# Optimization experiments

Hardware: AMD Instinct MI355X
Metric: run time of the kernel (lower is better)

Reference implementation:

```python
import jax, jax.numpy as jnp
import numpy as np


def _gcn_conv(x, W, b, src, dst, n):
    # x: [N, F_in] -> project first (dense GEMM), then normalized scatter-add.
    h = x @ W  # [N, F_out]
    deg = jax.ops.segment_sum(jnp.ones_like(dst, dtype=h.dtype), dst, num_segments=n)  # in-degree incl. self loops
    inv_sqrt = jax.lax.rsqrt(deg)  # deg >= 1 because self loops were added
    norm = inv_sqrt[src] * inv_sqrt[dst]  # [E+N]
    out = jax.ops.segment_sum(h[src] * norm[:, None], dst, num_segments=n)  # [N, F_out]
    return out + b


def setup_inputs() -> dict:
    key = jax.random.key(0)
    k1, k2, k3, k4 = jax.random.split(key, 4)
    N, E, F_IN, H, C = 10000, 160000, 3703, 1024, 6
    x = jax.random.normal(k1, (N, F_IN), dtype=jnp.float32)
    edge_index = jax.random.randint(k2, (2, E), 0, N, dtype=jnp.int64)
    # Glorot-style init for weights
    W1 = jax.random.normal(k3, (F_IN, H), dtype=jnp.float32) * np.float32(1.0 / np.sqrt(F_IN))
    W2 = jax.random.normal(k4, (H, C), dtype=jnp.float32) * np.float32(1.0 / np.sqrt(H))
    b1 = jnp.zeros((H,), dtype=jnp.float32)
    b2 = jnp.zeros((C,), dtype=jnp.float32)
    return {"x": x, "edge_index": edge_index, "W1": W1, "b1": b1, "W2": W2, "b2": b2}


def reference(x, edge_index, W1, b1, W2, b2):
    n = x.shape[0]
    # GCNConv adds self loops; degree normalization D^{-1/2}(A+I)D^{-1/2}
    loop = jnp.arange(n, dtype=edge_index.dtype)
    src = jnp.concatenate([edge_index[0], loop])
    dst = jnp.concatenate([edge_index[1], loop])
    h = _gcn_conv(x, W1, b1, src, dst, n)
    h = jax.nn.relu(h)
    # dropout is identity in eval mode
    h = _gcn_conv(h, W2, b2, src, dst, n)
    return jax.nn.log_softmax(h, axis=1)
```

## Files before the change

### kernel.cpp

```cpp
#include <hip/hip_runtime.h>
#include <stdint.h>

typedef unsigned short u16;
typedef unsigned int u32;
typedef __bf16 bf16x8 __attribute__((ext_vector_type(8)));
typedef float f32x4 __attribute__((ext_vector_type(4)));

#define N_NODES 10000
#define N_EDGES 160000
#define F_IN    3703
#define HDIM    1024
#define CDIM    6
#define MP      10112
#define KP      3712
#define KT      58

static __device__ __forceinline__ u16 f2bf(float f) {
    u32 u = __builtin_bit_cast(u32, f);
    u32 r = (u + 0x7fffu + ((u >> 16) & 1u)) >> 16;
    return (u16)r;
}
static __device__ __forceinline__ float bf2f(u16 b) {
    return __builtin_bit_cast(float, ((u32)b) << 16);
}

#define GL2LDS(g, l) __builtin_amdgcn_global_load_lds(                         \
    (const __attribute__((address_space(1))) void*)(g),                        \
    (__attribute__((address_space(3))) void*)(l), 16, 0, 0)

__global__ void k_count(const int* __restrict__ ei, int* counts) {
    int e = blockIdx.x * 256 + threadIdx.x;
    if (e < N_EDGES) {
        int dst = ei[N_EDGES + e];
        atomicAdd(&counts[dst], 1);
    }
}

__global__ void k_scan(const int* __restrict__ counts, int* __restrict__ offsets,
                       float* __restrict__ inv_sqrt) {
    __shared__ int sums[1024];
    int t = threadIdx.x;
    int local[10];
    int s = 0;
    #pragma unroll
    for (int i = 0; i < 10; i++) {
        int idx = t * 10 + i;
        int v = (idx < N_NODES) ? counts[idx] : 0;
        local[i] = s; s += v;
    }
    sums[t] = s;
    __syncthreads();
    for (int off = 1; off < 1024; off <<= 1) {
        int v = (t >= off) ? sums[t - off] : 0;
        __syncthreads();
        sums[t] += v;
        __syncthreads();
    }
    int base = (t == 0) ? 0 : sums[t - 1];
    #pragma unroll
    for (int i = 0; i < 10; i++) {
        int idx = t * 10 + i;
        if (idx < N_NODES) {
            offsets[idx] = base + local[i];
            inv_sqrt[idx] = rsqrtf((float)(counts[idx] + 1));
        }
    }
    if (t == 1023) offsets[N_NODES] = sums[1023];
}

__global__ void k_fill(const int* __restrict__ ei, const int* __restrict__ offsets,
                       int* cursor, int* __restrict__ edge_src) {
    int e = blockIdx.x * 256 + threadIdx.x;
    if (e < N_EDGES) {
        int src = ei[e];
        int dst = ei[N_EDGES + e];
        int pos = atomicAdd(&cursor[dst], 1);
        edge_src[offsets[dst] + pos] = src;
    }
}

__global__ void k_cvt_x(const float* __restrict__ x, u16* __restrict__ A) {
    const int KP4 = KP / 4;
    int i = blockIdx.x * 256 + threadIdx.x;
    if (i >= MP * KP4) return;
    int m = i / KP4;
    int k4 = (i - m * KP4) * 4;
    float v0 = 0.f, v1 = 0.f, v2 = 0.f, v3 = 0.f;
    if (m < N_NODES) {
        const float* xp = x + (size_t)m * F_IN;
        if (k4 + 3 < F_IN) {
            v0 = xp[k4]; v1 = xp[k4 + 1]; v2 = xp[k4 + 2]; v3 = xp[k4 + 3];
        } else {
            if (k4     < F_IN) v0 = xp[k4];
            if (k4 + 1 < F_IN) v1 = xp[k4 + 1];
            if (k4 + 2 < F_IN) v2 = xp[k4 + 2];
            if (k4 + 3 < F_IN) v3 = xp[k4 + 3];
        }
    }
    ushort4 o;
    o.x = f2bf(v0); o.y = f2bf(v1); o.z = f2bf(v2); o.w = f2bf(v3);
    *(ushort4*)&A[(size_t)m * KP + k4] = o;
}

__global__ void k_cvt_w1t(const float* __restrict__ W1, u16* __restrict__ BT) {
    __shared__ u16 tile[64][66];
    int k0 = blockIdx.x * 64, n0 = blockIdx.y * 64;
    int tx = threadIdx.x & 63, ty = threadIdx.x >> 6;
    #pragma unroll
    for (int i = 0; i < 16; i++) {
        int kk = ty + i * 4;
        int k = k0 + kk;
        float v = (k < F_IN) ? W1[(size_t)k * HDIM + n0 + tx] : 0.f;
        tile[kk][tx] = f2bf(v);
    }
    __syncthreads();
    #pragma unroll
    for (int i = 0; i < 16; i++) {
        int nn = ty + i * 4;
        BT[(size_t)(n0 + nn) * KP + k0 + tx] = tile[tx][nn];
    }
}

__global__ __launch_bounds__(256) void k_gemm1(const u16* __restrict__ A,
                                               const u16* __restrict__ BT,
                                               u16* __restrict__ H1) {
    __shared__ __align__(16) u16 As[128 * 64];
    __shared__ __align__(16) u16 Bs[128 * 64];
    const int tid = threadIdx.x;
    const int lane = tid & 63;
    const int wid = tid >> 6;
    const int wm = wid >> 1, wn = wid & 1;

    const u32 orig = (u32)blockIdx.y * 8u + (u32)blockIdx.x;
    const u32 lin  = (orig & 7u) * 79u + (orig >> 3);
    const int bm = (int)(lin >> 3);
    const int bn = (int)(lin & 7u);

    int srow[4], scol[4], sdst[4];
    #pragma unroll
    for (int j = 0; j < 4; j++) {
        int q = wid * 4 + j;
        int e = q * 512 + lane * 8;
        int row = e >> 6, c = e & 63;
        srow[j] = row;
        scol[j] = c ^ ((row & 7) << 3);
        sdst[j] = q * 512;
    }
    const u16* Abase = A + (size_t)bm * 128 * KP;
    const u16* Bbase = BT + (size_t)bn * 128 * KP;

    f32x4 acc[4][4];
    #pragma unroll
    for (int i = 0; i < 4; i++)
        #pragma unroll
        for (int j = 0; j < 4; j++)
            acc[i][j] = (f32x4)0.f;

    for (int kt = 0; kt < KT; ++kt) {
        const int k0 = kt * 64;
        #pragma unroll
        for (int j = 0; j < 4; j++)
            GL2LDS(Abase + srow[j] * KP + k0 + scol[j], As + sdst[j]);
        #pragma unroll
        for (int j = 0; j < 4; j++)
            GL2LDS(Bbase + srow[j] * KP + k0 + scol[j], Bs + sdst[j]);
        __syncthreads();

        const int rA = wm * 64 + (lane & 15);
        const int rB = wn * 64 + (lane & 15);
        const int cb = (lane >> 4) << 3;
        #pragma unroll
        for (int kk = 0; kk < 2; kk++) {
            bf16x8 av[4], bv[4];
            const int cc = kk * 32 + cb;
            #pragma unroll
            for (int i = 0; i < 4; i++) {
                int r = rA + i * 16;
                av[i] = *(const bf16x8*)(As + r * 64 + (cc ^ ((r & 7) << 3)));
                int r2 = rB + i * 16;
                bv[i] = *(const bf16x8*)(Bs + r2 * 64 + (cc ^ ((r2 & 7) << 3)));
            }
            #pragma unroll
            for (int i = 0; i < 4; i++)
                #pragma unroll
                for (int j = 0; j < 4; j++)
                    acc[i][j] = __builtin_amdgcn_mfma_f32_16x16x32_bf16(
                        av[i], bv[j], acc[i][j], 0, 0, 0);
        }
        __syncthreads();
    }

    const int cr = (lane >> 4) * 4;
    const int ccol = lane & 15;
    #pragma unroll
    for (int i = 0; i < 4; i++) {
        #pragma unroll
        for (int j = 0; j < 4; j++) {
            #pragma unroll
            for (int r = 0; r < 4; r++) {
                int row = bm * 128 + wm * 64 + i * 16 + cr + r;
                if (row < N_NODES) {
                    int col = bn * 128 + wn * 64 + j * 16 + ccol;
                    H1[(size_t)row * HDIM + col] = f2bf(acc[i][j][r]);
                }
            }
        }
    }
}

__global__ void k_agg1g2(const u16* __restrict__ H1, const int* __restrict__ offsets,
                         const int* __restrict__ edge_src, const float* __restrict__ inv_sqrt,
                         const float* __restrict__ b1, const float* __restrict__ W2,
                         float* __restrict__ H2) {
    __shared__ float red[4][8];
    int node = blockIdx.x;
    int t = threadIdx.x;
    int f = t * 4;
    float is_n = inv_sqrt[node];
    float a0, a1, a2, a3;
    {
        float w = is_n * is_n;
        ushort4 v = *(const ushort4*)(H1 + (size_t)node * HDIM + f);
        a0 = bf2f(v.x) * w; a1 = bf2f(v.y) * w; a2 = bf2f(v.z) * w; a3 = bf2f(v.w) * w;
    }
    int beg = offsets[node], end = offsets[node + 1];
    for (int e = beg; e < end; ++e) {
        int s = edge_src[e];
        float w = inv_sqrt[s] * is_n;
        ushort4 v = *(const ushort4*)(H1 + (size_t)s * HDIM + f);
        a0 += bf2f(v.x) * w; a1 += bf2f(v.y) * w; a2 += bf2f(v.z) * w; a3 += bf2f(v.w) * w;
    }
    float4 bb = *(const float4*)(b1 + f);
    float z0 = fmaxf(a0 + bb.x, 0.f);
    float z1 = fmaxf(a1 + bb.y, 0.f);
    float z2 = fmaxf(a2 + bb.z, 0.f);
    float z3 = fmaxf(a3 + bb.w, 0.f);
    float acc[6];
    #pragma unroll
    for (int c = 0; c < 6; c++)
        acc[c] = z0 * W2[(size_t)f * 6 + c] + z1 * W2[(size_t)(f + 1) * 6 + c]
               + z2 * W2[(size_t)(f + 2) * 6 + c] + z3 * W2[(size_t)(f + 3) * 6 + c];
    #pragma unroll
    for (int c = 0; c < 6; c++) {
        #pragma unroll
        for (int off = 32; off > 0; off >>= 1) acc[c] += __shfl_xor(acc[c], off);
    }
    int lane = t & 63, wv = t >> 6;
    if (lane == 0) {
        #pragma unroll
        for (int c = 0; c < 6; c++) red[wv][c] = acc[c];
    }
    __syncthreads();
    if (t < 6) {
        float s = red[0][t] + red[1][t] + red[2][t] + red[3][t];
        H2[(size_t)node * CDIM + t] = s;
    }
}

__global__ void k_agg2(const float* __restrict__ H2, const int* __restrict__ offsets,
                       const int* __restrict__ edge_src, const float* __restrict__ inv_sqrt,
                       const float* __restrict__ b2, float* __restrict__ out) {
    int gt = blockIdx.x * 256 + threadIdx.x;
    int node = gt >> 3, sub = gt & 7;
    if (node >= N_NODES) return;
    float is_n = inv_sqrt[node];
    float acc[6] = {0.f, 0.f, 0.f, 0.f, 0.f, 0.f};
    int beg = offsets[node], end = offsets[node + 1];
    for (int e = beg + sub; e < end; e += 8) {
        int s = edge_src[e];
        float w = inv_sqrt[s] * is_n;
        #pragma unroll
        for (int c = 0; c < 6; c++) acc[c] += H2[(size_t)s * CDIM + c] * w;
    }
    if (sub == 0) {
        float w = is_n * is_n;
        #pragma unroll
        for (int c = 0; c < 6; c++) acc[c] += H2[(size_t)node * CDIM + c] * w;
    }
    #pragma unroll
    for (int off = 1; off < 8; off <<= 1) {
        #pragma unroll
        for (int c = 0; c < 6; c++) acc[c] += __shfl_xor(acc[c], off);
    }
    if (sub == 0) {
        float z[6];
        #pragma unroll
        for (int c = 0; c < 6; c++) z[c] = acc[c] + b2[c];
        float m = z[0];
        #pragma unroll
        for (int c = 1; c < 6; c++) m = fmaxf(m, z[c]);
        float ssum = 0.f;
        #pragma unroll
        for (int c = 0; c < 6; c++) ssum += __expf(z[c] - m);
        float l = m + logf(ssum);
        #pragma unroll
        for (int c = 0; c < 6; c++) out[(size_t)node * CDIM + c] = z[c] - l;
    }
}

extern "C" void kernel_launch(void* const* d_in, const int* in_sizes, int n_in,
                              void* d_out, int out_size, void* d_ws, size_t ws_size,
                              hipStream_t stream) {
    const float* x  = (const float*)d_in[0];
    const int*   ei = (const int*)d_in[1];
    const float* W1 = (const float*)d_in[2];
    const float* b1 = (const float*)d_in[3];
    const float* W2 = (const float*)d_in[4];
    const float* b2 = (const float*)d_in[5];
    float* out = (float*)d_out;

    char* ws = (char*)d_ws;
    size_t off = 0;
    auto alloc = [&](size_t bytes) -> void* {
        void* p = ws + off;
        off += (bytes + 255) & ~(size_t)255;
        return p;
    };
    u16* A        = (u16*)alloc((size_t)MP * KP * 2);
    u16* BT       = (u16*)alloc((size_t)HDIM * KP * 2);
    u16* H1       = (u16*)alloc((size_t)N_NODES * HDIM * 2);
    int* counts   = (int*)alloc(N_NODES * 4);
    int* cursor   = (int*)alloc(N_NODES * 4);
    int* offsets  = (int*)alloc((N_NODES + 1) * 4);
    float* inv_sq = (float*)alloc(N_NODES * 4);
    int* edge_src = (int*)alloc(N_EDGES * 4);
    float* H2 = (float*)BT;

    hipMemsetAsync(counts, 0, N_NODES * 4, stream);
    hipMemsetAsync(cursor, 0, N_NODES * 4, stream);
    k_count<<<(N_EDGES + 255) / 256, 256, 0, stream>>>(ei, counts);
    k_scan<<<1, 1024, 0, stream>>>(counts, offsets, inv_sq);
    k_fill<<<(N_EDGES + 255) / 256, 256, 0, stream>>>(ei, offsets, cursor, edge_src);

    k_cvt_x<<<(MP * (KP / 4) + 255) / 256, 256, 0, stream>>>(x, A);
    dim3 gT(KP / 64, HDIM / 64);
    k_cvt_w1t<<<gT, 256, 0, stream>>>(W1, BT);

    dim3 gG(HDIM / 128, MP / 128);
    k_gemm1<<<gG, 256, 0, stream>>>(A, BT, H1);

    k_agg1g2<<<N_NODES, 256, 0, stream>>>(H1, offsets, edge_src, inv_sq, b1, W2, H2);
    k_agg2<<<(N_NODES * 8 + 255) / 256, 256, 0, stream>>>(H2, offsets, edge_src, inv_sq, b2, out);
}
```

Measured before the change: 240.1 us.

## Fuse fp32-to-bf16 conversion of x into GEMM with double-buffered LDS pipeline

Drops the separate pass that converts x to padded bf16. The GEMM now loads fp32 x directly into registers, converts it, and writes it into a double-buffered LDS tile. The next k-tile's A and B loads are issued before the current tile's MFMAs, so global latency overlaps with compute. The block scan is rewritten to use wavefront shuffles instead of a barrier-heavy LDS Hillis-Steele scan. In exchange, fp32 A loads are unaligned (F_IN is odd), use more registers and double LDS use, which may lower occupancy, and x is re-read by all 8 column blocks at fp32 width.

After: 287.5 us. 19.7% more time.

```diff
diff --git a/kernel.cpp b/kernel.cpp
--- a/kernel.cpp
+++ b/kernel.cpp
@@ -5,13 +5,13 @@
 typedef unsigned int u32;
 typedef __bf16 bf16x8 __attribute__((ext_vector_type(8)));
 typedef float f32x4 __attribute__((ext_vector_type(4)));
+typedef float f32x4u __attribute__((ext_vector_type(4), aligned(4)));
 
 #define N_NODES 10000
 #define N_EDGES 160000
 #define F_IN    3703
 #define HDIM    1024
 #define CDIM    6
-#define MP      10112
 #define KP      3712
 #define KT      58
 
@@ -38,8 +38,8 @@
 
 __global__ void k_scan(const int* __restrict__ counts, int* __restrict__ offsets,
                        float* __restrict__ inv_sqrt) {
-    __shared__ int sums[1024];
-    int t = threadIdx.x;
+    __shared__ int wsum[16];
+    int t = threadIdx.x, lane = t & 63, wv = t >> 6;
     int local[10];
     int s = 0;
     #pragma unroll
@@ -48,15 +48,21 @@
         int v = (idx < N_NODES) ? counts[idx] : 0;
         local[i] = s; s += v;
     }
-    sums[t] = s;
-    __syncthreads();
-    for (int off = 1; off < 1024; off <<= 1) {
-        int v = (t >= off) ? sums[t - off] : 0;
-        __syncthreads();
-        sums[t] += v;
-        __syncthreads();
-    }
-    int base = (t == 0) ? 0 : sums[t - 1];
+    int incl = s;
+    #pragma unroll
+    for (int off = 1; off < 64; off <<= 1) {
+        int v = __shfl_up(incl, off);
+        if (lane >= off) incl += v;
+    }
+    if (lane == 63) wsum[wv] = incl;
+    __syncthreads();
+    if (t == 0) {
+        int a = 0;
+        #pragma unroll
+        for (int i = 0; i < 16; i++) { int v = wsum[i]; wsum[i] = a; a += v; }
+    }
+    __syncthreads();
+    int base = wsum[wv] + incl - s;
     #pragma unroll
     for (int i = 0; i < 10; i++) {
         int idx = t * 10 + i;
@@ -65,7 +71,7 @@
             inv_sqrt[idx] = rsqrtf((float)(counts[idx] + 1));
         }
     }
-    if (t == 1023) offsets[N_NODES] = sums[1023];
+    if (t == 1023) offsets[N_NODES] = wsum[15] + incl;
 }
 
 __global__ void k_fill(const int* __restrict__ ei, const int* __restrict__ offsets,
@@ -79,29 +85,6 @@
     }
 }
 
-__global__ void k_cvt_x(const float* __restrict__ x, u16* __restrict__ A) {
-    const int KP4 = KP / 4;
-    int i = blockIdx.x * 256 + threadIdx.x;
-    if (i >= MP * KP4) return;
-    int m = i / KP4;
-    int k4 = (i - m * KP4) * 4;
-    float v0 = 0.f, v1 = 0.f, v2 = 0.f, v3 = 0.f;
-    if (m < N_NODES) {
-        const float* xp = x + (size_t)m * F_IN;
-        if (k4 + 3 < F_IN) {
-            v0 = xp[k4]; v1 = xp[k4 + 1]; v2 = xp[k4 + 2]; v3 = xp[k4 + 3];
-        } else {
-            if (k4     < F_IN) v0 = xp[k4];
-            if (k4 + 1 < F_IN) v1 = xp[k4 + 1];
-            if (k4 + 2 < F_IN) v2 = xp[k4 + 2];
-            if (k4 + 3 < F_IN) v3 = xp[k4 + 3];
-        }
-    }
-    ushort4 o;
-    o.x = f2bf(v0); o.y = f2bf(v1); o.z = f2bf(v2); o.w = f2bf(v3);
-    *(ushort4*)&A[(size_t)m * KP + k4] = o;
-}
-
 __global__ void k_cvt_w1t(const float* __restrict__ W1, u16* __restrict__ BT) {
     __shared__ u16 tile[64][66];
     int k0 = blockIdx.x * 64, n0 = blockIdx.y * 64;
@@ -121,11 +104,11 @@
     }
 }
 
-__global__ __launch_bounds__(256) void k_gemm1(const u16* __restrict__ A,
+__global__ __launch_bounds__(256) void k_gemm1(const float* __restrict__ x,
                                                const u16* __restrict__ BT,
                                                u16* __restrict__ H1) {
-    __shared__ __align__(16) u16 As[128 * 64];
-    __shared__ __align__(16) u16 Bs[128 * 64];
+    __shared__ __align__(16) u16 As[2][128 * 64];
+    __shared__ __align__(16) u16 Bs[2][128 * 64];
     const int tid = threadIdx.x;
     const int lane = tid & 63;
     const int wid = tid >> 6;
@@ -136,18 +119,20 @@
     const int bm = (int)(lin >> 3);
     const int bn = (int)(lin & 7u);
 
-    int srow[4], scol[4], sdst[4];
+    int srowB[4], scolB[4], sdstB[4];
     #pragma unroll
     for (int j = 0; j < 4; j++) {
         int q = wid * 4 + j;
         int e = q * 512 + lane * 8;
         int row = e >> 6, c = e & 63;
-        srow[j] = row;
-        scol[j] = c ^ ((row & 7) << 3);
-        sdst[j] = q * 512;
-    }
-    const u16* Abase = A + (size_t)bm * 128 * KP;
+        srowB[j] = row;
+        scolB[j] = c ^ ((row & 7) << 3);
+        sdstB[j] = q * 512;
+    }
     const u16* Bbase = BT + (size_t)bn * 128 * KP;
+
+    const int ar0 = tid >> 4;
+    const int ac0 = (tid & 15) * 4;
 
     f32x4 acc[4][4];
     #pragma unroll
@@ -156,16 +141,58 @@
         for (int j = 0; j < 4; j++)
             acc[i][j] = (f32x4)0.f;
 
+    f32x4u va[8];
+    auto loadA = [&](int kt) {
+        const int k4 = kt * 64 + ac0;
+        #pragma unroll
+        for (int p = 0; p < 8; p++) {
+            int m = bm * 128 + ar0 + p * 16;
+            f32x4u v = {0.f, 0.f, 0.f, 0.f};
+            if (m < N_NODES) {
+                const float* xp = x + (size_t)m * F_IN + k4;
+                if (k4 + 4 <= F_IN) {
+                    v = *(const f32x4u*)xp;
+                } else {
+                    if (k4     < F_IN) v.x = xp[0];
+                    if (k4 + 1 < F_IN) v.y = xp[1];
+                    if (k4 + 2 < F_IN) v.z = xp[2];
+                }
+            }
+            va[p] = v;
+        }
+    };
+    auto writeA = [&](int buf) {
+        #pragma unroll
+        for (int p = 0; p < 8; p++) {
+            int r = ar0 + p * 16;
+            int c = ac0 ^ ((r & 7) << 3);
+            ushort4 o;
+            o.x = f2bf(va[p].x); o.y = f2bf(va[p].y);
+            o.z = f2bf(va[p].z); o.w = f2bf(va[p].w);
+            *(ushort4*)&As[buf][r * 64 + c] = o;
+        }
+    };
+
+    loadA(0);
+    #pragma unroll
+    for (int j = 0; j < 4; j++)
+        GL2LDS(Bbase + (size_t)srowB[j] * KP + 0 + scolB[j], &Bs[0][sdstB[j]]);
+    writeA(0);
+    __syncthreads();
+
+    int cur = 0;
     for (int kt = 0; kt < KT; ++kt) {
-        const int k0 = kt * 64;
-        #pragma unroll
-        for (int j = 0; j < 4; j++)
-            GL2LDS(Abase + srow[j] * KP + k0 + scol[j], As + sdst[j]);
-        #pragma unroll
-        for (int j = 0; j < 4; j++)
-            GL2LDS(Bbase + srow[j] * KP + k0 + scol[j], Bs + sdst[j]);
-        __syncthreads();
-
+        const bool has_next = (kt + 1 < KT);
+        if (has_next) {
+            loadA(kt + 1);
+            const int k0n = (kt + 1) * 64;
+            #pragma unroll
+            for (int j = 0; j < 4; j++)
+                GL2LDS(Bbase + (size_t)srowB[j] * KP + k0n + scolB[j], &Bs[cur ^ 1][sdstB[j]]);
+        }
+
+        const u16* as = As[cur];
+        const u16* bs = Bs[cur];
         const int rA = wm * 64 + (lane & 15);
         const int rB = wn * 64 + (lane & 15);
         const int cb = (lane >> 4) << 3;
@@ -176,9 +203,9 @@
             #pragma unroll
             for (int i = 0; i < 4; i++) {
                 int r = rA + i * 16;
-                av[i] = *(const bf16x8*)(As + r * 64 + (cc ^ ((r & 7) << 3)));
+                av[i] = *(const bf16x8*)(as + r * 64 + (cc ^ ((r & 7) << 3)));
                 int r2 = rB + i * 16;
-                bv[i] = *(const bf16x8*)(Bs + r2 * 64 + (cc ^ ((r2 & 7) << 3)));
+                bv[i] = *(const bf16x8*)(bs + r2 * 64 + (cc ^ ((r2 & 7) << 3)));
             }
             #pragma unroll
             for (int i = 0; i < 4; i++)
@@ -187,7 +214,10 @@
                     acc[i][j] = __builtin_amdgcn_mfma_f32_16x16x32_bf16(
                         av[i], bv[j], acc[i][j], 0, 0, 0);
         }
+
+        if (has_next) writeA(cur ^ 1);
         __syncthreads();
+        cur ^= 1;
     }
 
     const int cr = (lane >> 4) * 4;
@@ -316,7 +346,6 @@
         off += (bytes + 255) & ~(size_t)255;
         return p;
     };
-    u16* A        = (u16*)alloc((size_t)MP * KP * 2);
     u16* BT       = (u16*)alloc((size_t)HDIM * KP * 2);
     u16* H1       = (u16*)alloc((size_t)N_NODES * HDIM * 2);
     int* counts   = (int*)alloc(N_NODES * 4);
@@ -332,12 +361,11 @@
     k_scan<<<1, 1024, 0, stream>>>(counts, offsets, inv_sq);
     k_fill<<<(N_EDGES + 255) / 256, 256, 0, stream>>>(ei, offsets, cursor, edge_src);
 
-    k_cvt_x<<<(MP * (KP / 4) + 255) / 256, 256, 0, stream>>>(x, A);
     dim3 gT(KP / 64, HDIM / 64);
     k_cvt_w1t<<<gT, 256, 0, stream>>>(W1, BT);
 
-    dim3 gG(HDIM / 128, MP / 128);
-    k_gemm1<<<gG, 256, 0, stream>>>(A, BT, H1);
+    dim3 gG(HDIM / 128, 79);
+    k_gemm1<<<gG, 256, 0, stream>>>(x, BT, H1);
 
     k_agg1g2<<<N_NODES, 256, 0, stream>>>(H1, offsets, edge_src, inv_sq, b1, W2, H2);
     k_agg2<<<(N_NODES * 8 + 255) / 256, 256, 0, stream>>>(H2, offsets, edge_src, inv_sq, b2, out);
```
